# Performance work log

Measured on AMD Instinct MI355X. Metric: run time of the kernel, lower is better.

The kernel has to match this reference:

```python
import jax, jax.numpy as jnp
import numpy as np

K_HOPS = 3
NUM_GRAPHS = 64
GN_EPS = 1e-5


def setup_inputs() -> dict:
    key = jax.random.key(0)
    ks = jax.random.split(key, 6)
    N, E, F = 50000, 625000, 128
    y = jax.random.normal(ks[0], (N, F), dtype=jnp.float32)
    edge_index = jax.random.randint(ks[1], (2, E), 0, N, dtype=jnp.int64)
    edge_weight = jax.random.uniform(ks[2], (E,), dtype=jnp.float32)
    batch = jnp.sort(jax.random.randint(ks[3], (N,), 0, NUM_GRAPHS, dtype=jnp.int64))
    tag_w = jax.random.normal(ks[4], (K_HOPS + 1, F, F), dtype=jnp.float32) * (1.0 / np.sqrt(F))
    tag_b = jnp.zeros((F,), dtype=jnp.float32)
    gn_weight = jnp.ones((F,), dtype=jnp.float32)
    gn_bias = jnp.zeros((F,), dtype=jnp.float32)
    gn_mean_scale = jnp.ones((F,), dtype=jnp.float32)
    return {"y": y, "edge_index": edge_index, "edge_weight": edge_weight,
            "batch": batch, "tag_w": tag_w, "tag_b": tag_b,
            "gn_weight": gn_weight, "gn_bias": gn_bias, "gn_mean_scale": gn_mean_scale}


def reference(y, edge_index, edge_weight, batch, tag_w, tag_b, gn_weight, gn_bias, gn_mean_scale):
    N = y.shape[0]
    src, dst = edge_index[0], edge_index[1]

    # --- TAGConv: symmetric gcn_norm (no self-loops), K hops ---
    deg = jax.ops.segment_sum(edge_weight, dst, num_segments=N)  # [N]
    dinv = jnp.where(deg > 0, jax.lax.rsqrt(jnp.maximum(deg, 1e-30)), 0.0)
    norm = dinv[src] * edge_weight * dinv[dst]  # [E]

    h = y
    out = h @ tag_w[0]
    for k in range(1, K_HOPS + 1):
        # one hop of message passing: gather from src, scatter-sum at dst
        h = jax.ops.segment_sum(norm[:, None] * h[src], dst, num_segments=N)  # [N,F]
        out = out + h @ tag_w[k]
    out = out + tag_b

    # --- GraphNorm over per-graph segments ---
    cnt = jax.ops.segment_sum(jnp.ones((N,), out.dtype), batch, num_segments=NUM_GRAPHS)
    cnt = jnp.maximum(cnt, 1.0)[:, None]  # [G,1]
    mean = jax.ops.segment_sum(out, batch, num_segments=NUM_GRAPHS) / cnt  # [G,F]
    xc = out - gn_mean_scale * mean[batch]
    var = jax.ops.segment_sum(xc * xc, batch, num_segments=NUM_GRAPHS) / cnt  # [G,F]
    hn = gn_weight * xc * jax.lax.rsqrt(var[batch] + GN_EPS) + gn_bias

    # --- activation; dropout is identity in eval mode; residual ---
    h_act = jax.nn.relu(hn)
    return y + h_act
```

## Files before the change

kernel.cpp:

```cpp
#include <hip/hip_runtime.h>

#define F 128
#define GRAPHS 64
#define GN_EPS 1e-5f
#define PB 256

typedef short short8 __attribute__((ext_vector_type(8)));
typedef float f32x4 __attribute__((ext_vector_type(4)));

__device__ __forceinline__ unsigned short f2b(float f) {
    unsigned u = __float_as_uint(f);
    unsigned r = (u + 0x7fffu + ((u >> 16) & 1u)) >> 16;
    return (unsigned short)r;
}
__device__ __forceinline__ float b2f(unsigned short h) {
    return __uint_as_float(((unsigned)h) << 16);
}

struct MArgs {
    const float* y; const int* ei; const float* ew; const int* batch;
    const float* tw; const float* tb; const float* gnw; const float* gnb; const float* gms;
    float* res;
    float* S1; float* S2; int* gstart; float* dinv; int* offs; int* hist_t; int* bbase;
    uint2* part; unsigned* csr; unsigned short* Wf; unsigned short* hcat; unsigned short* outb;
    int N, E, NB, chunk, fb, gb;
    size_t NF;
};

__global__ __launch_bounds__(256) void k_prep(MArgs a) {
    __shared__ int hist[256];
    const int t0 = 256;
    const int t1 = t0 + a.fb;
    const int t2 = t1 + 256;
    const int t3 = t2 + a.gb;
    int tid = threadIdx.x;
    int task = blockIdx.x;
    if (task < t0) {
        hist[tid] = 0;
        __syncthreads();
        int e0 = task * a.chunk, e1 = min(e0 + a.chunk, a.E);
        for (int e = e0 + tid; e < e1; e += 256)
            atomicAdd(&hist[a.ei[a.E + e] >> 8], 1);
        __syncthreads();
        for (int k = tid; k < a.NB; k += 256)
            a.hist_t[k * PB + task] = hist[k];
    } else if (task < t1) {
        int i = (task - t0) * 256 + tid;
        if (i < a.N * 32) {
            float4 v = ((const float4*)a.y)[i];
            ((ushort4*)a.hcat)[i] = make_ushort4(f2b(v.x), f2b(v.y), f2b(v.z), f2b(v.w));
        }
    } else if (task < t2) {
        int i = (task - t1) * 256 + tid;
        int seg = i >> 14;
        int r = i & 16383;
        int kb = r >> 12;
        int wcc = (r >> 11) & 1;
        int ntt = (r >> 9) & 3;
        int lane = (r >> 3) & 63;
        int j = i & 7;
        int k = kb * 32 + (lane >> 4) * 8 + j;
        int nn = wcc * 64 + ntt * 16 + (lane & 15);
        a.Wf[i] = f2b(a.tw[seg * 16384 + k * 128 + nn]);
    } else if (task < t3) {
        int i = (task - t2) * 256 + tid;
        if (i < a.N) {
            int bb = a.batch[i];
            if (i == 0) {
                for (int g = 0; g <= bb; ++g) a.gstart[g] = 0;
            } else {
                int bp = a.batch[i - 1];
                for (int g = bp + 1; g <= bb; ++g) a.gstart[g] = i;
            }
            if (i == a.N - 1) {
                for (int g = bb + 1; g <= GRAPHS; ++g) a.gstart[g] = a.N;
            }
        }
    } else {
        int z = task - t3;
        float* dst = a.S1 + z * 2048;
        for (int i2 = tid; i2 < 2048; i2 += 256) dst[i2] = 0.f;
    }
}

__global__ __launch_bounds__(256) void k_part(MArgs a) {
    __shared__ int cur[256];
    __shared__ int rs[256];
    int t = threadIdx.x;
    int k = blockIdx.x;
    int total = 0, pref = 0;
    if (t < a.NB) {
        const int4* row = (const int4*)(a.hist_t + t * PB);
        for (int q = 0; q < PB / 4; ++q) {
            int4 v = row[q];
            int c4 = q * 4;
            total += v.x + v.y + v.z + v.w;
            if (c4 + 4 <= k) pref += v.x + v.y + v.z + v.w;
            else {
                if (c4 + 0 < k) pref += v.x;
                if (c4 + 1 < k) pref += v.y;
                if (c4 + 2 < k) pref += v.z;
                if (c4 + 3 < k) pref += v.w;
            }
        }
    }
    rs[t] = (t < a.NB) ? total : 0;
    __syncthreads();
    for (int off = 1; off < 256; off <<= 1) {
        int x = (t >= off) ? rs[t - off] : 0;
        __syncthreads();
        rs[t] += x;
        __syncthreads();
    }
    int rowStart = (t > 0) ? rs[t - 1] : 0;
    cur[t] = rowStart + pref;
    if (k == 0 && t <= a.NB) a.bbase[t] = rowStart;
    __syncthreads();
    int e0 = k * a.chunk, e1 = min(e0 + a.chunk, a.E);
    for (int e = e0 + t; e < e1; e += 256) {
        int dst = a.ei[a.E + e];
        int src = a.ei[e];
        float w = a.ew[e];
        int slot = atomicAdd(&cur[dst >> 8], 1);
        a.part[slot] = make_uint2(((unsigned)dst << 16) | (unsigned)src, __float_as_uint(w));
    }
}

__global__ __launch_bounds__(256) void k_bucket(MArgs a) {
    __shared__ float degf[256];
    __shared__ int cnte[256];
    __shared__ int scn[256];
    __shared__ int cur2[256];
    int t = threadIdx.x;
    int b = blockIdx.x;
    degf[t] = 0.f;
    cnte[t] = 0;
    __syncthreads();
    int s0 = a.bbase[b];
    int s1 = a.bbase[b + 1];
    for (int i = s0 + t; i < s1; i += 256) {
        uint2 pp = a.part[i];
        int dl = (pp.x >> 16) & 255;
        atomicAdd(&degf[dl], __uint_as_float(pp.y));
        atomicAdd(&cnte[dl], 1);
    }
    __syncthreads();
    int v = cnte[t];
    scn[t] = v;
    __syncthreads();
    for (int off = 1; off < 256; off <<= 1) {
        int x = (t >= off) ? scn[t - off] : 0;
        __syncthreads();
        scn[t] += x;
        __syncthreads();
    }
    int node = b * 256 + t;
    int base = s0 + scn[t] - v;
    if (node < a.N) {
        float d = degf[t];
        a.dinv[node] = (d > 0.f) ? rsqrtf(fmaxf(d, 1e-30f)) : 0.f;
        a.offs[node] = base;
    }
    if (b == 0 && t == 0) a.offs[a.N] = a.E;
    cur2[t] = base;
    __syncthreads();
    for (int i = s0 + t; i < s1; i += 256) {
        uint2 pp = a.part[i];
        int dl = (pp.x >> 16) & 255;
        unsigned src = pp.x & 0xffffu;
        int slot = atomicAdd(&cur2[dl], 1);
        a.csr[slot] = (src << 16) | (unsigned)f2b(__uint_as_float(pp.y));
    }
}

template<bool FIX>
__device__ void ph_hop(const MArgs& a, const unsigned short* __restrict__ hin,
                       unsigned short* __restrict__ hout) {
    int lane = threadIdx.x & 63;
    int wv = threadIdx.x >> 6;
    int gq = lane >> 4, fl = lane & 15;
    int node = blockIdx.x * 4 + wv;
    if (node >= a.N) return;
    int e0 = a.offs[node], e1 = a.offs[node + 1];
    float acc[8] = {};
    for (int j = e0; j < e1; j += 16) {
        int base = j + gq * 4;
        int c0 = min(base + 0, e1 - 1), c1 = min(base + 1, e1 - 1);
        int c2 = min(base + 2, e1 - 1), c3 = min(base + 3, e1 - 1);
        unsigned ed0 = a.csr[c0], ed1 = a.csr[c1], ed2 = a.csr[c2], ed3 = a.csr[c3];
        float w0 = (base + 0 < e1) ? b2f((unsigned short)(ed0 & 0xffffu)) : 0.f;
        float w1 = (base + 1 < e1) ? b2f((unsigned short)(ed1 & 0xffffu)) : 0.f;
        float w2 = (base + 2 < e1) ? b2f((unsigned short)(ed2 & 0xffffu)) : 0.f;
        float w3 = (base + 3 < e1) ? b2f((unsigned short)(ed3 & 0xffffu)) : 0.f;
        if (FIX) {
            w0 *= a.dinv[ed0 >> 16];
            w1 *= a.dinv[ed1 >> 16];
            w2 *= a.dinv[ed2 >> 16];
            w3 *= a.dinv[ed3 >> 16];
        }
        short8 h0 = *(const short8*)(hin + (size_t)(ed0 >> 16) * 128 + fl * 8);
        short8 h1 = *(const short8*)(hin + (size_t)(ed1 >> 16) * 128 + fl * 8);
        short8 h2 = *(const short8*)(hin + (size_t)(ed2 >> 16) * 128 + fl * 8);
        short8 h3 = *(const short8*)(hin + (size_t)(ed3 >> 16) * 128 + fl * 8);
        if (FIX && fl < 4) {
            int wi = base + fl;
            if (wi < e1) {
                float wf2 = (fl == 0) ? w0 : (fl == 1) ? w1 : (fl == 2) ? w2 : w3;
                unsigned ede = (fl == 0) ? ed0 : (fl == 1) ? ed1 : (fl == 2) ? ed2 : ed3;
                a.csr[wi] = (ede & 0xffff0000u) | (unsigned)f2b(wf2);
            }
        }
        #pragma unroll
        for (int k = 0; k < 8; ++k) {
            acc[k] += w0 * b2f((unsigned short)h0[k]) + w1 * b2f((unsigned short)h1[k]);
            acc[k] += w2 * b2f((unsigned short)h2[k]) + w3 * b2f((unsigned short)h3[k]);
        }
    }
    #pragma unroll
    for (int k = 0; k < 8; ++k) {
        acc[k] += __shfl_xor(acc[k], 16);
        acc[k] += __shfl_xor(acc[k], 32);
    }
    if (lane < 16) {
        float dd = a.dinv[node];
        short8 o;
        #pragma unroll
        for (int k = 0; k < 8; ++k) o[k] = (short)f2b(acc[k] * dd);
        *(short8*)(hout + (size_t)node * 128 + fl * 8) = o;
    }
}

template<int H>
__global__ __launch_bounds__(256) void k_hop(MArgs a) {
    const unsigned short* hin = a.hcat + (size_t)(H - 1) * a.NF;
    unsigned short* hout = a.hcat + (size_t)H * a.NF;
    if constexpr (H == 1) ph_hop<true>(a, hin, hout);
    else ph_hop<false>(a, hin, hout);
}

__global__ __launch_bounds__(256) void k_gemm(MArgs a) {
    __shared__ unsigned short As[2][4096];
    const unsigned short* __restrict__ hcat = a.hcat;
    const unsigned short* __restrict__ Wf = a.Wf;
    const float* bias = a.tb;
    int M = a.N;
    size_t NF = a.NF;
    int lane = threadIdx.x & 63;
    int wid = threadIdx.x >> 6;
    int wr = wid & 1, wc = wid >> 1;
    int quad = lane >> 4, l15 = lane & 15;
    int row0 = blockIdx.x * 64;
    f32x4 acc[2][4] = {};
    for (int s = 0; s < 4; ++s) {
        const unsigned short* Aseg = hcat + (size_t)s * NF;
        short8 stg[4];
        #pragma unroll
        for (int i = 0; i < 4; ++i) {
            int flat = (wc * 4 + i) * 64 + lane;
            int r = flat >> 4, c = flat & 15;
            stg[i] = *(const short8*)(Aseg + (size_t)(row0 + wr * 32 + r) * 128 + c * 8);
        }
        __syncthreads();
        #pragma unroll
        for (int i = 0; i < 4; ++i) {
            int flat = (wc * 4 + i) * 64 + lane;
            int r = flat >> 4, c = flat & 15;
            *(short8*)&As[wr][(r * 16 + (c ^ (r & 15))) * 8] = stg[i];
        }
        __syncthreads();
        #pragma unroll
        for (int kb = 0; kb < 4; ++kb) {
            int swz = ((kb * 4 + quad) ^ l15) * 8;
            short8 a0 = *(short8*)&As[wr][l15 * 128 + swz];
            short8 a1 = *(short8*)&As[wr][(16 + l15) * 128 + swz];
            const unsigned short* bb = Wf + (size_t)(((s * 4 + kb) * 2 + wc) * 4) * 512 + lane * 8;
            short8 b0 = *(const short8*)(bb + 0 * 512);
            short8 b1 = *(const short8*)(bb + 1 * 512);
            short8 b2 = *(const short8*)(bb + 2 * 512);
            short8 b3 = *(const short8*)(bb + 3 * 512);
            acc[0][0] = __builtin_amdgcn_mfma_f32_16x16x32_bf16(a0, b0, acc[0][0], 0, 0, 0);
            acc[0][1] = __builtin_amdgcn_mfma_f32_16x16x32_bf16(a0, b1, acc[0][1], 0, 0, 0);
            acc[0][2] = __builtin_amdgcn_mfma_f32_16x16x32_bf16(a0, b2, acc[0][2], 0, 0, 0);
            acc[0][3] = __builtin_amdgcn_mfma_f32_16x16x32_bf16(a0, b3, acc[0][3], 0, 0, 0);
            acc[1][0] = __builtin_amdgcn_mfma_f32_16x16x32_bf16(a1, b0, acc[1][0], 0, 0, 0);
            acc[1][1] = __builtin_amdgcn_mfma_f32_16x16x32_bf16(a1, b1, acc[1][1], 0, 0, 0);
            acc[1][2] = __builtin_amdgcn_mfma_f32_16x16x32_bf16(a1, b2, acc[1][2], 0, 0, 0);
            acc[1][3] = __builtin_amdgcn_mfma_f32_16x16x32_bf16(a1, b3, acc[1][3], 0, 0, 0);
        }
    }

    float bcol[4];
    #pragma unroll
    for (int nt = 0; nt < 4; ++nt) bcol[nt] = bias[wc * 64 + nt * 16 + l15];
    int rg[2][4];
    #pragma unroll
    for (int mt = 0; mt < 2; ++mt) {
        #pragma unroll
        for (int r = 0; r < 4; ++r) {
            int row = row0 + wr * 32 + mt * 16 + quad * 4 + r;
            rg[mt][r] = (row < M) ? a.batch[row] : -1;
            if (row < M) {
                #pragma unroll
                for (int nt = 0; nt < 4; ++nt) {
                    float vv = acc[mt][nt][r] + bcol[nt];
                    a.outb[(size_t)row * 128 + wc * 64 + nt * 16 + l15] = f2b(vv);
                }
            }
        }
    }
    int glo = a.batch[row0];
    int ghi = a.batch[min(row0 + 63, M - 1)];
    for (int g = glo; g <= ghi; ++g) {
        float s1[4] = {0.f, 0.f, 0.f, 0.f}, s2[4] = {0.f, 0.f, 0.f, 0.f};
        #pragma unroll
        for (int mt = 0; mt < 2; ++mt) {
            #pragma unroll
            for (int r = 0; r < 4; ++r) {
                if (rg[mt][r] == g) {
                    #pragma unroll
                    for (int nt = 0; nt < 4; ++nt) {
                        float vv = acc[mt][nt][r] + bcol[nt];
                        s1[nt] += vv;
                        s2[nt] += vv * vv;
                    }
                }
            }
        }
        #pragma unroll
        for (int nt = 0; nt < 4; ++nt) {
            s1[nt] += __shfl_xor(s1[nt], 16);
            s1[nt] += __shfl_xor(s1[nt], 32);
            s2[nt] += __shfl_xor(s2[nt], 16);
            s2[nt] += __shfl_xor(s2[nt], 32);
        }
        if (quad == 0) {
            #pragma unroll
            for (int nt = 0; nt < 4; ++nt) {
                int col = wc * 64 + nt * 16 + l15;
                atomicAdd(&a.S1[g * 128 + col], s1[nt]);
                atomicAdd(&a.S2[g * 128 + col], s2[nt]);
            }
        }
    }
}

__global__ __launch_bounds__(256) void k_final(MArgs a) {
    int total = a.N * 32;
    const ushort4* yb = (const ushort4*)a.hcat;
    const ushort4* ob = (const ushort4*)a.outb;
    float4* res = (float4*)a.res;
    int idx = blockIdx.x * 256 + threadIdx.x;
    if (idx >= total) return;
    int node = idx >> 5;
    int q = idx & 31;
    int g = a.batch[node];
    float rc = 1.f / fmaxf((float)(a.gstart[g + 1] - a.gstart[g]), 1.f);
    int base = g * 128 + q * 4;
    float4 s1 = *(const float4*)&a.S1[base];
    float4 s2 = *(const float4*)&a.S2[base];
    float4 w  = *(const float4*)&a.gnw[q * 4];
    float4 bb = *(const float4*)&a.gnb[q * 4];
    float4 sc = *(const float4*)&a.gms[q * 4];
    ushort4 yv = yb[idx];
    ushort4 ov = ob[idx];
    float4 r;
    {
        float m = s1.x * rc, e2 = s2.x * rc, s = sc.x;
        float var = e2 - (2.f * s - s * s) * m * m;
        float A = w.x * rsqrtf(var + GN_EPS);
        r.x = b2f(yv.x) + fmaxf(0.f, (b2f(ov.x) - s * m) * A + bb.x);
    }
    {
        float m = s1.y * rc, e2 = s2.y * rc, s = sc.y;
        float var = e2 - (2.f * s - s * s) * m * m;
        float A = w.y * rsqrtf(var + GN_EPS);
        r.y = b2f(yv.y) + fmaxf(0.f, (b2f(ov.y) - s * m) * A + bb.y);
    }
    {
        float m = s1.z * rc, e2 = s2.z * rc, s = sc.z;
        float var = e2 - (2.f * s - s * s) * m * m;
        float A = w.z * rsqrtf(var + GN_EPS);
        r.z = b2f(yv.z) + fmaxf(0.f, (b2f(ov.z) - s * m) * A + bb.z);
    }
    {
        float m = s1.w * rc, e2 = s2.w * rc, s = sc.w;
        float var = e2 - (2.f * s - s * s) * m * m;
        float A = w.w * rsqrtf(var + GN_EPS);
        r.w = b2f(yv.w) + fmaxf(0.f, (b2f(ov.w) - s * m) * A + bb.w);
    }
    res[idx] = r;
}

extern "C" void kernel_launch(void* const* d_in, const int* in_sizes, int n_in,
                              void* d_out, int out_size, void* d_ws, size_t ws_size,
                              hipStream_t stream) {
    const float* y     = (const float*)d_in[0];
    const int*   ei    = (const int*)d_in[1];
    const float* ew    = (const float*)d_in[2];
    const int*   batch = (const int*)d_in[3];
    const float* tag_w = (const float*)d_in[4];
    const float* tag_b = (const float*)d_in[5];
    const float* gnw   = (const float*)d_in[6];
    const float* gnb   = (const float*)d_in[7];
    const float* gms   = (const float*)d_in[8];

    const int N = in_sizes[0] / F;
    const int E = in_sizes[1] / 2;
    const size_t NF = (size_t)N * F;
    const int NB = (N + 255) >> 8;
    const int NH = NB * PB;
    const int chunk = (E + PB - 1) / PB;
    const int fb = (N * 32 + 255) / 256;
    const int gb = (N + 255) / 256;

    char* p = (char*)d_ws;
    float* S1 = (float*)p;       p += (size_t)GRAPHS * F * 4;
    float* S2 = (float*)p;       p += (size_t)GRAPHS * F * 4;
    int*   gstart = (int*)p;     p += 512;
    float* dinv = (float*)p;     p += (size_t)N * 4;
    int*   offs = (int*)p;       p += (size_t)(N + 4) * 4;
    int*   hist_t = (int*)p;     p += (size_t)NH * 4;
    int*   bbase = (int*)p;      p += 1040;
    uint2* part = (uint2*)p;     p += (size_t)E * 8;
    unsigned* csr = (unsigned*)p; p += (size_t)E * 4;
    unsigned short* Wf = (unsigned short*)p; p += 4 * 128 * 128 * 2;
    unsigned short* hcat = (unsigned short*)p; p += NF * 2 * 4;
    unsigned short* outb = (unsigned short*)p; p += NF * 2;
    p += 4096;

    MArgs ha;
    ha.y = y; ha.ei = ei; ha.ew = ew; ha.batch = batch;
    ha.tw = tag_w; ha.tb = tag_b; ha.gnw = gnw; ha.gnb = gnb; ha.gms = gms;
    ha.res = (float*)d_out;
    ha.S1 = S1; ha.S2 = S2; ha.gstart = gstart; ha.dinv = dinv; ha.offs = offs;
    ha.hist_t = hist_t; ha.bbase = bbase; ha.part = part; ha.csr = csr;
    ha.Wf = Wf; ha.hcat = hcat; ha.outb = outb;
    ha.N = N; ha.E = E; ha.NB = NB; ha.chunk = chunk; ha.fb = fb; ha.gb = gb;
    ha.NF = NF;

    k_prep<<<256 + fb + 256 + gb + 8, 256, 0, stream>>>(ha);
    k_part<<<PB, 256, 0, stream>>>(ha);
    k_bucket<<<NB, 256, 0, stream>>>(ha);
    k_hop<1><<<(N + 3) / 4, 256, 0, stream>>>(ha);
    k_hop<2><<<(N + 3) / 4, 256, 0, stream>>>(ha);
    k_hop<3><<<(N + 3) / 4, 256, 0, stream>>>(ha);
    k_gemm<<<(N + 63) / 64, 256, 0, stream>>>(ha);
    k_final<<<(N * 32 + 255) / 256, 256, 0, stream>>>(ha);
}
```

Baseline: 230.1 us.

## Replace bucketed CSR build with atomic histogram, fuse third hop into GEMM

The two-pass bucket partition (per-chunk histograms, partition into an intermediate buffer, per-bucket CSR) is replaced by three kernels: global atomic degree and count histogram, block scan with an atomic global base, and atomic scatter into CSR with the symmetric norm precomputed per edge. This removes the dinv fix-up pass from hop 1. The third hop is computed inside the GEMM kernel, written straight to shared memory as the fourth A segment, which saves one launch and an N×F bf16 write and read. CSR rows are no longer in node order, and the global atomics on dst may contend, so memory locality and determinism change.

```diff
diff --git a/kernel.cpp b/kernel.cpp
--- a/kernel.cpp
+++ b/kernel.cpp
@@ -3,7 +3,6 @@
 #define F 128
 #define GRAPHS 64
 #define GN_EPS 1e-5f
-#define PB 256
 
 typedef short short8 __attribute__((ext_vector_type(8)));
 typedef float f32x4 __attribute__((ext_vector_type(4)));
@@ -21,37 +20,27 @@
     const float* y; const int* ei; const float* ew; const int* batch;
     const float* tw; const float* tb; const float* gnw; const float* gnb; const float* gms;
     float* res;
-    float* S1; float* S2; int* gstart; float* dinv; int* offs; int* hist_t; int* bbase;
-    uint2* part; unsigned* csr; unsigned short* Wf; unsigned short* hcat; unsigned short* outb;
-    int N, E, NB, chunk, fb, gb;
+    float* S1; float* S2; int* gcur; float* deg; int* cnt;
+    int* gstart; float* dinv; int* offs; int* cur;
+    unsigned* csr; unsigned short* Wf; unsigned short* hcat; unsigned short* outb;
+    int N, E, NB, fb, gb, zb, zn4;
     size_t NF;
 };
 
 __global__ __launch_bounds__(256) void k_prep(MArgs a) {
-    __shared__ int hist[256];
-    const int t0 = 256;
-    const int t1 = t0 + a.fb;
-    const int t2 = t1 + 256;
-    const int t3 = t2 + a.gb;
+    const int t0 = a.fb;
+    const int t1 = t0 + 256;
+    const int t2 = t1 + a.gb;
     int tid = threadIdx.x;
     int task = blockIdx.x;
     if (task < t0) {
-        hist[tid] = 0;
-        __syncthreads();
-        int e0 = task * a.chunk, e1 = min(e0 + a.chunk, a.E);
-        for (int e = e0 + tid; e < e1; e += 256)
-            atomicAdd(&hist[a.ei[a.E + e] >> 8], 1);
-        __syncthreads();
-        for (int k = tid; k < a.NB; k += 256)
-            a.hist_t[k * PB + task] = hist[k];
-    } else if (task < t1) {
-        int i = (task - t0) * 256 + tid;
+        int i = task * 256 + tid;
         if (i < a.N * 32) {
             float4 v = ((const float4*)a.y)[i];
             ((ushort4*)a.hcat)[i] = make_ushort4(f2b(v.x), f2b(v.y), f2b(v.z), f2b(v.w));
         }
-    } else if (task < t2) {
-        int i = (task - t1) * 256 + tid;
+    } else if (task < t1) {
+        int i = (task - t0) * 256 + tid;
         int seg = i >> 14;
         int r = i & 16383;
         int kb = r >> 12;
@@ -62,8 +51,8 @@
         int k = kb * 32 + (lane >> 4) * 8 + j;
         int nn = wcc * 64 + ntt * 16 + (lane & 15);
         a.Wf[i] = f2b(a.tw[seg * 16384 + k * 128 + nn]);
-    } else if (task < t3) {
-        int i = (task - t2) * 256 + tid;
+    } else if (task < t2) {
+        int i = (task - t1) * 256 + tid;
         if (i < a.N) {
             int bb = a.batch[i];
             if (i == 0) {
@@ -77,76 +66,27 @@
             }
         }
     } else {
-        int z = task - t3;
-        float* dst = a.S1 + z * 2048;
-        for (int i2 = tid; i2 < 2048; i2 += 256) dst[i2] = 0.f;
-    }
-}
-
-__global__ __launch_bounds__(256) void k_part(MArgs a) {
-    __shared__ int cur[256];
-    __shared__ int rs[256];
+        int i4 = (task - t2) * 256 + tid;
+        if (i4 < a.zn4) ((float4*)a.S1)[i4] = make_float4(0.f, 0.f, 0.f, 0.f);
+    }
+}
+
+__global__ __launch_bounds__(256) void k_hist(MArgs a) {
+    int e = blockIdx.x * 256 + threadIdx.x;
+    if (e >= a.E) return;
+    int dst = a.ei[a.E + e];
+    float w = a.ew[e];
+    atomicAdd(&a.deg[dst], w);
+    atomicAdd(&a.cnt[dst], 1);
+}
+
+__global__ __launch_bounds__(256) void k_offs(MArgs a) {
+    __shared__ int scn[256];
+    __shared__ int base;
     int t = threadIdx.x;
-    int k = blockIdx.x;
-    int total = 0, pref = 0;
-    if (t < a.NB) {
-        const int4* row = (const int4*)(a.hist_t + t * PB);
-        for (int q = 0; q < PB / 4; ++q) {
-            int4 v = row[q];
-            int c4 = q * 4;
-            total += v.x + v.y + v.z + v.w;
-            if (c4 + 4 <= k) pref += v.x + v.y + v.z + v.w;
-            else {
-                if (c4 + 0 < k) pref += v.x;
-                if (c4 + 1 < k) pref += v.y;
-                if (c4 + 2 < k) pref += v.z;
-                if (c4 + 3 < k) pref += v.w;
-            }
-        }
-    }
-    rs[t] = (t < a.NB) ? total : 0;
-    __syncthreads();
-    for (int off = 1; off < 256; off <<= 1) {
-        int x = (t >= off) ? rs[t - off] : 0;
-        __syncthreads();
-        rs[t] += x;
-        __syncthreads();
-    }
-    int rowStart = (t > 0) ? rs[t - 1] : 0;
-    cur[t] = rowStart + pref;
-    if (k == 0 && t <= a.NB) a.bbase[t] = rowStart;
-    __syncthreads();
-    int e0 = k * a.chunk, e1 = min(e0 + a.chunk, a.E);
-    for (int e = e0 + t; e < e1; e += 256) {
-        int dst = a.ei[a.E + e];
-        int src = a.ei[e];
-        float w = a.ew[e];
-        int slot = atomicAdd(&cur[dst >> 8], 1);
-        a.part[slot] = make_uint2(((unsigned)dst << 16) | (unsigned)src, __float_as_uint(w));
-    }
-}
-
-__global__ __launch_bounds__(256) void k_bucket(MArgs a) {
-    __shared__ float degf[256];
-    __shared__ int cnte[256];
-    __shared__ int scn[256];
-    __shared__ int cur2[256];
-    int t = threadIdx.x;
-    int b = blockIdx.x;
-    degf[t] = 0.f;
-    cnte[t] = 0;
-    __syncthreads();
-    int s0 = a.bbase[b];
-    int s1 = a.bbase[b + 1];
-    for (int i = s0 + t; i < s1; i += 256) {
-        uint2 pp = a.part[i];
-        int dl = (pp.x >> 16) & 255;
-        atomicAdd(&degf[dl], __uint_as_float(pp.y));
-        atomicAdd(&cnte[dl], 1);
-    }
-    __syncthreads();
-    int v = cnte[t];
-    scn[t] = v;
+    int node = blockIdx.x * 256 + t;
+    int c = (node < a.N) ? a.cnt[node] : 0;
+    scn[t] = c;
     __syncthreads();
     for (int off = 1; off < 256; off <<= 1) {
         int x = (t >= off) ? scn[t - off] : 0;
@@ -154,34 +94,38 @@
         scn[t] += x;
         __syncthreads();
     }
-    int node = b * 256 + t;
-    int base = s0 + scn[t] - v;
+    if (t == 255) base = atomicAdd(a.gcur, scn[255]);
+    __syncthreads();
     if (node < a.N) {
-        float d = degf[t];
+        int off = base + scn[t] - c;
+        a.offs[node] = off;
+        a.cur[node] = off;
+        float d = a.deg[node];
         a.dinv[node] = (d > 0.f) ? rsqrtf(fmaxf(d, 1e-30f)) : 0.f;
-        a.offs[node] = base;
-    }
-    if (b == 0 && t == 0) a.offs[a.N] = a.E;
-    cur2[t] = base;
-    __syncthreads();
-    for (int i = s0 + t; i < s1; i += 256) {
-        uint2 pp = a.part[i];
-        int dl = (pp.x >> 16) & 255;
-        unsigned src = pp.x & 0xffffu;
-        int slot = atomicAdd(&cur2[dl], 1);
-        a.csr[slot] = (src << 16) | (unsigned)f2b(__uint_as_float(pp.y));
-    }
-}
-
-template<bool FIX>
-__device__ void ph_hop(const MArgs& a, const unsigned short* __restrict__ hin,
-                       unsigned short* __restrict__ hout) {
+    }
+}
+
+__global__ __launch_bounds__(256) void k_scatter(MArgs a) {
+    int e = blockIdx.x * 256 + threadIdx.x;
+    if (e >= a.E) return;
+    int dst = a.ei[a.E + e];
+    int src = a.ei[e];
+    float w = a.ew[e];
+    float wf = a.dinv[src] * w * a.dinv[dst];
+    int slot = atomicAdd(&a.cur[dst], 1);
+    a.csr[slot] = ((unsigned)src << 16) | (unsigned)f2b(wf);
+}
+
+__device__ __forceinline__ void ph_hop(const MArgs& a,
+                                       const unsigned short* __restrict__ hin,
+                                       unsigned short* __restrict__ hout) {
     int lane = threadIdx.x & 63;
     int wv = threadIdx.x >> 6;
     int gq = lane >> 4, fl = lane & 15;
     int node = blockIdx.x * 4 + wv;
     if (node >= a.N) return;
-    int e0 = a.offs[node], e1 = a.offs[node + 1];
+    int e0 = a.offs[node];
+    int e1 = e0 + a.cnt[node];
     float acc[8] = {};
     for (int j = e0; j < e1; j += 16) {
         int base = j + gq * 4;
@@ -192,24 +136,10 @@
         float w1 = (base + 1 < e1) ? b2f((unsigned short)(ed1 & 0xffffu)) : 0.f;
         float w2 = (base + 2 < e1) ? b2f((unsigned short)(ed2 & 0xffffu)) : 0.f;
         float w3 = (base + 3 < e1) ? b2f((unsigned short)(ed3 & 0xffffu)) : 0.f;
-        if (FIX) {
-            w0 *= a.dinv[ed0 >> 16];
-            w1 *= a.dinv[ed1 >> 16];
-            w2 *= a.dinv[ed2 >> 16];
-            w3 *= a.dinv[ed3 >> 16];
-        }
         short8 h0 = *(const short8*)(hin + (size_t)(ed0 >> 16) * 128 + fl * 8);
         short8 h1 = *(const short8*)(hin + (size_t)(ed1 >> 16) * 128 + fl * 8);
         short8 h2 = *(const short8*)(hin + (size_t)(ed2 >> 16) * 128 + fl * 8);
         short8 h3 = *(const short8*)(hin + (size_t)(ed3 >> 16) * 128 + fl * 8);
-        if (FIX && fl < 4) {
-            int wi = base + fl;
-            if (wi < e1) {
-                float wf2 = (fl == 0) ? w0 : (fl == 1) ? w1 : (fl == 2) ? w2 : w3;
-                unsigned ede = (fl == 0) ? ed0 : (fl == 1) ? ed1 : (fl == 2) ? ed2 : ed3;
-                a.csr[wi] = (ede & 0xffff0000u) | (unsigned)f2b(wf2);
-            }
-        }
         #pragma unroll
         for (int k = 0; k < 8; ++k) {
             acc[k] += w0 * b2f((unsigned short)h0[k]) + w1 * b2f((unsigned short)h1[k]);
@@ -222,25 +152,23 @@
         acc[k] += __shfl_xor(acc[k], 32);
     }
     if (lane < 16) {
-        float dd = a.dinv[node];
         short8 o;
         #pragma unroll
-        for (int k = 0; k < 8; ++k) o[k] = (short)f2b(acc[k] * dd);
+        for (int k = 0; k < 8; ++k) o[k] = (short)f2b(acc[k]);
         *(short8*)(hout + (size_t)node * 128 + fl * 8) = o;
     }
 }
 
 template<int H>
 __global__ __launch_bounds__(256) void k_hop(MArgs a) {
-    const unsigned short* hin = a.hcat + (size_t)(H - 1) * a.NF;
-    unsigned short* hout = a.hcat + (size_t)H * a.NF;
-    if constexpr (H == 1) ph_hop<true>(a, hin, hout);
-    else ph_hop<false>(a, hin, hout);
-}
-
-__global__ __launch_bounds__(256) void k_gemm(MArgs a) {
+    ph_hop(a, a.hcat + (size_t)(H - 1) * a.NF, a.hcat + (size_t)H * a.NF);
+}
+
+__global__ __launch_bounds__(256) void k_hopgemm(MArgs a) {
     __shared__ unsigned short As[2][4096];
+    __shared__ unsigned short As3[2][4096];
     const unsigned short* __restrict__ hcat = a.hcat;
+    const unsigned short* __restrict__ hs2 = a.hcat + 2 * a.NF;
     const unsigned short* __restrict__ Wf = a.Wf;
     const float* bias = a.tb;
     int M = a.N;
@@ -250,29 +178,71 @@
     int wr = wid & 1, wc = wid >> 1;
     int quad = lane >> 4, l15 = lane & 15;
     int row0 = blockIdx.x * 64;
+
+    {
+        int qd = lane >> 4, fl = lane & 15;
+        for (int it = 0; it < 4; ++it) {
+            int ndl = wid * 16 + qd * 4 + it;
+            int nd = row0 + ndl;
+            float acc[8] = {};
+            if (nd < M) {
+                int e0 = a.offs[nd];
+                int len = a.cnt[nd];
+                int e1 = e0 + len;
+                for (int j = e0; j < e1; j += 4) {
+                    int c0 = min(j + 0, e1 - 1), c1 = min(j + 1, e1 - 1);
+                    int c2 = min(j + 2, e1 - 1), c3 = min(j + 3, e1 - 1);
+                    unsigned ed0 = a.csr[c0], ed1 = a.csr[c1];
+                    unsigned ed2 = a.csr[c2], ed3 = a.csr[c3];
+                    float w0 = (j + 0 < e1) ? b2f((unsigned short)(ed0 & 0xffffu)) : 0.f;
+                    float w1 = (j + 1 < e1) ? b2f((unsigned short)(ed1 & 0xffffu)) : 0.f;
+                    float w2 = (j + 2 < e1) ? b2f((unsigned short)(ed2 & 0xffffu)) : 0.f;
+                    float w3 = (j + 3 < e1) ? b2f((unsigned short)(ed3 & 0xffffu)) : 0.f;
+                    short8 h0 = *(const short8*)(hs2 + (size_t)(ed0 >> 16) * 128 + fl * 8);
+                    short8 h1 = *(const short8*)(hs2 + (size_t)(ed1 >> 16) * 128 + fl * 8);
+                    short8 h2 = *(const short8*)(hs2 + (size_t)(ed2 >> 16) * 128 + fl * 8);
+                    short8 h3 = *(const short8*)(hs2 + (size_t)(ed3 >> 16) * 128 + fl * 8);
+                    #pragma unroll
+                    for (int k = 0; k < 8; ++k) {
+                        acc[k] += w0 * b2f((unsigned short)h0[k]) + w1 * b2f((unsigned short)h1[k]);
+                        acc[k] += w2 * b2f((unsigned short)h2[k]) + w3 * b2f((unsigned short)h3[k]);
+                    }
+                }
+            }
+            short8 o;
+            #pragma unroll
+            for (int k = 0; k < 8; ++k) o[k] = (short)f2b(acc[k]);
+            int wrH = ndl >> 5, rr = ndl & 31;
+            *(short8*)&As3[wrH][(rr * 16 + (fl ^ (rr & 15))) * 8] = o;
+        }
+    }
+
     f32x4 acc[2][4] = {};
     for (int s = 0; s < 4; ++s) {
-        const unsigned short* Aseg = hcat + (size_t)s * NF;
-        short8 stg[4];
-        #pragma unroll
-        for (int i = 0; i < 4; ++i) {
-            int flat = (wc * 4 + i) * 64 + lane;
-            int r = flat >> 4, c = flat & 15;
-            stg[i] = *(const short8*)(Aseg + (size_t)(row0 + wr * 32 + r) * 128 + c * 8);
-        }
-        __syncthreads();
-        #pragma unroll
-        for (int i = 0; i < 4; ++i) {
-            int flat = (wc * 4 + i) * 64 + lane;
-            int r = flat >> 4, c = flat & 15;
-            *(short8*)&As[wr][(r * 16 + (c ^ (r & 15))) * 8] = stg[i];
-        }
-        __syncthreads();
+        if (s < 3) {
+            const unsigned short* Aseg = hcat + (size_t)s * NF;
+            short8 stg[4];
+            #pragma unroll
+            for (int i = 0; i < 4; ++i) {
+                int flat = (wc * 4 + i) * 64 + lane;
+                int r = flat >> 4, c = flat & 15;
+                stg[i] = *(const short8*)(Aseg + (size_t)(row0 + wr * 32 + r) * 128 + c * 8);
+            }
+            __syncthreads();
+            #pragma unroll
+            for (int i = 0; i < 4; ++i) {
+                int flat = (wc * 4 + i) * 64 + lane;
+                int r = flat >> 4, c = flat & 15;
+                *(short8*)&As[wr][(r * 16 + (c ^ (r & 15))) * 8] = stg[i];
+            }
+            __syncthreads();
+        }
+        const unsigned short* AsP = (s < 3) ? As[wr] : As3[wr];
         #pragma unroll
         for (int kb = 0; kb < 4; ++kb) {
             int swz = ((kb * 4 + quad) ^ l15) * 8;
-            short8 a0 = *(short8*)&As[wr][l15 * 128 + swz];
-            short8 a1 = *(short8*)&As[wr][(16 + l15) * 128 + swz];
+            short8 a0 = *(const short8*)&AsP[l15 * 128 + swz];
+            short8 a1 = *(const short8*)&AsP[(16 + l15) * 128 + swz];
             const unsigned short* bb = Wf + (size_t)(((s * 4 + kb) * 2 + wc) * 4) * 512 + lane * 8;
             short8 b0 = *(const short8*)(bb + 0 * 512);
             short8 b1 = *(const short8*)(bb + 1 * 512);
@@ -408,42 +378,46 @@
     const int E = in_sizes[1] / 2;
     const size_t NF = (size_t)N * F;
     const int NB = (N + 255) >> 8;
-    const int NH = NB * PB;
-    const int chunk = (E + PB - 1) / PB;
     const int fb = (N * 32 + 255) / 256;
     const int gb = (N + 255) / 256;
 
     char* p = (char*)d_ws;
     float* S1 = (float*)p;       p += (size_t)GRAPHS * F * 4;
     float* S2 = (float*)p;       p += (size_t)GRAPHS * F * 4;
+    int*   gcur = (int*)p;       p += 4096;
+    float* deg = (float*)p;      p += (size_t)N * 4;
+    int*   cnt = (int*)p;        p += (size_t)N * 4;
+    size_t zeroBytes = (size_t)(p - (char*)d_ws);
     int*   gstart = (int*)p;     p += 512;
     float* dinv = (float*)p;     p += (size_t)N * 4;
-    int*   offs = (int*)p;       p += (size_t)(N + 4) * 4;
-    int*   hist_t = (int*)p;     p += (size_t)NH * 4;
-    int*   bbase = (int*)p;      p += 1040;
-    uint2* part = (uint2*)p;     p += (size_t)E * 8;
+    int*   offs = (int*)p;       p += (size_t)N * 4;
+    int*   cur  = (int*)p;       p += (size_t)N * 4;
     unsigned* csr = (unsigned*)p; p += (size_t)E * 4;
     unsigned short* Wf = (unsigned short*)p; p += 4 * 128 * 128 * 2;
-    unsigned short* hcat = (unsigned short*)p; p += NF * 2 * 4;
+    unsigned short* hcat = (unsigned short*)p; p += NF * 2 * 3;
     unsigned short* outb = (unsigned short*)p; p += NF * 2;
     p += 4096;
+
+    const int zn4 = (int)(zeroBytes / 16);
+    const int zb = (zn4 + 255) / 256;
 
     MArgs ha;
     ha.y = y; ha.ei = ei; ha.ew = ew; ha.batch = batch;
     ha.tw = tag_w; ha.tb = tag_b; ha.gnw = gnw; ha.gnb = gnb; ha.gms = gms;
     ha.res = (float*)d_out;
-    ha.S1 = S1; ha.S2 = S2; ha.gstart = gstart; ha.dinv = dinv; ha.offs = offs;
-    ha.hist_t = hist_t; ha.bbase = bbase; ha.part = part; ha.csr = csr;
-    ha.Wf = Wf; ha.hcat = hcat; ha.outb = outb;
-    ha.N = N; ha.E = E; ha.NB = NB; ha.chunk = chunk; ha.fb = fb; ha.gb = gb;
+    ha.S1 = S1; ha.S2 = S2; ha.gcur = gcur; ha.deg = deg; ha.cnt = cnt;
+    ha.gstart = gstart; ha.dinv = dinv; ha.offs = offs; ha.cur = cur;
+    ha.csr = csr; ha.Wf = Wf; ha.hcat = hcat; ha.outb = outb;
+    ha.N = N; ha.E = E; ha.NB = NB; ha.fb = fb; ha.gb = gb; ha.zb = zb; ha.zn4 = zn4;
     ha.NF = NF;
 
-    k_prep<<<256 + fb + 256 + gb + 8, 256, 0, stream>>>(ha);
-    k_part<<<PB, 256, 0, stream>>>(ha);
-    k_bucket<<<NB, 256, 0, stream>>>(ha);
+    const int eb = (E + 255) / 256;
+    k_prep<<<fb + 256 + gb + zb, 256, 0, stream>>>(ha);
+    k_hist<<<eb, 256, 0, stream>>>(ha);
+    k_offs<<<NB, 256, 0, stream>>>(ha);
+    k_scatter<<<eb, 256, 0, stream>>>(ha);
     k_hop<1><<<(N + 3) / 4, 256, 0, stream>>>(ha);
     k_hop<2><<<(N + 3) / 4, 256, 0, stream>>>(ha);
-    k_hop<3><<<(N + 3) / 4, 256, 0, stream>>>(ha);
-    k_gemm<<<(N + 63) / 64, 256, 0, stream>>>(ha);
+    k_hopgemm<<<(N + 63) / 64, 256, 0, stream>>>(ha);
     k_final<<<(N * 32 + 255) / 256, 256, 0, stream>>>(ha);
 }
```

After: 317.2 us. +37.8%, slower.
